# Optimization experiments

Measured on AMD Instinct MI355X. Metric: run time of the kernel, lower is better.

The kernel has to match this reference:

```python
import jax, jax.numpy as jnp
import numpy as np

G, NPG, C, H, F, L = 256, 128, 16, 128, 128, 3
N = G * NPG          # 32768 nodes
E = 524288           # 16 edges per node on average
REG, REG_C = 0.01, 0.01
LN_EPS = 1e-5


def setup_inputs() -> dict:
    key = jax.random.key(0)
    ks = jax.random.split(key, 20)
    x = jax.random.normal(ks[0], (N, F), dtype=jnp.float32)
    # edges kept within each graph so dense pooling matches to_dense_batch semantics
    epg = E // G
    offs = jnp.repeat(jnp.arange(G, dtype=jnp.int64) * NPG, epg)
    src = jax.random.randint(ks[1], (E,), 0, NPG, dtype=jnp.int64) + offs
    tgt = jax.random.randint(ks[2], (E,), 0, NPG, dtype=jnp.int64) + offs
    edge_index = jnp.stack([src, tgt])
    mask_breaks = jax.random.bernoulli(ks[3], 0.5, (E,))
    s = jax.random.uniform(ks[4], (N, C), dtype=jnp.float32)
    batch = jnp.repeat(jnp.arange(G, dtype=jnp.int64), NPG)
    sc = 1.0 / np.sqrt(H)
    Wn = jax.random.normal(ks[5], (L, H, H), dtype=jnp.float32) * sc
    bn_ = jax.random.normal(ks[6], (L, H), dtype=jnp.float32) * sc
    Wo = jax.random.normal(ks[7], (L, H, H), dtype=jnp.float32) * sc
    bo = jax.random.normal(ks[8], (L, H), dtype=jnp.float32) * sc
    Wr = jax.random.normal(ks[9], (L, H, H), dtype=jnp.float32) * sc
    ln_g = jnp.ones((L, H), dtype=jnp.float32)
    ln_b = jnp.zeros((L, H), dtype=jnp.float32)
    fln_g = jnp.ones((H,), dtype=jnp.float32)
    fln_b = jnp.zeros((H,), dtype=jnp.float32)
    lin_w = jax.random.normal(ks[10], (1, H), dtype=jnp.float32) * sc
    bias = jnp.zeros((1,), dtype=jnp.float32)
    return {"x": x, "edge_index": edge_index, "mask_breaks": mask_breaks, "s": s,
            "batch": batch, "Wn": Wn, "bn_": bn_, "Wo": Wo, "bo": bo, "Wr": Wr,
            "ln_g": ln_g, "ln_b": ln_b, "fln_g": fln_g, "fln_b": fln_b,
            "lin_w": lin_w, "bias": bias}


def _layernorm(h, g, b):
    mu = jnp.mean(h, axis=-1, keepdims=True)
    v = jnp.mean(jnp.square(h - mu), axis=-1, keepdims=True)
    return (h - mu) * jax.lax.rsqrt(v + LN_EPS) * g + b


def reference(x, edge_index, mask_breaks, s, batch, Wn, bn_, Wo, bo, Wr,
              ln_g, ln_b, fln_g, fln_b, lin_w, bias):
    src, tgt = edge_index[0], edge_index[1]
    ones_e = jnp.ones((E,), dtype=x.dtype)
    cnt = jax.ops.segment_sum(ones_e, tgt, num_segments=N)          # in-degree
    inv_cnt = (1.0 / jnp.maximum(cnt, 1.0))[:, None]
    h = x
    for i in range(L):
        x_in = h @ Wn[i].T + bn_[i]
        x_out = h @ Wo[i].T + bo[i]
        x_root = h @ Wr[i].T
        msg = jnp.where(mask_breaks[:, None], x_in[src], x_out[src])  # [E,H]
        agg = jax.ops.segment_sum(msg, tgt, num_segments=N) * inv_cnt  # mean aggr
        h = jax.nn.relu(_layernorm(agg + x_root, ln_g[i], ln_b[i]))
    # dense per-graph views (equal-size graphs, batch ids sorted -> reshape)
    xd = h.reshape(G, NPG, H)
    sd = s.reshape(G, NPG, C)
    pooled = jnp.einsum("gnc,gnh->gch", sd, xd)                      # [G,C,H]
    pooled = _layernorm(pooled, fln_g, fln_b)
    xc = pooled @ lin_w.T                                            # [G,C,1]
    col_sum = sd.sum(axis=1)                                          # [G,C]
    cmask = (col_sum > 0)[..., None]
    xc = xc * cmask.astype(xc.dtype)
    out = xc.sum(axis=1) + bias                                      # [G,1]
    reg_loss = jnp.abs(Wo).sum() + jnp.abs(bo).sum()
    denom = (cmask.astype(xc.dtype).squeeze(-1) + 1e-7).sum(axis=1, keepdims=True)
    l1_loss = (jnp.abs(xc).sum(axis=1) / denom).mean()
    losses = REG * reg_loss + REG_C * l1_loss
    return out, losses, xc
```

## Files before the change

kernel.cpp:

```cpp
#include <hip/hip_runtime.h>

#define NN   32768
#define HD   128
#define EE   524288
#define GG   256
#define EPG  2048
#define CCd  16
#define LLd  3

typedef short short8 __attribute__((ext_vector_type(8)));
typedef float f32x4 __attribute__((ext_vector_type(4)));

__device__ __forceinline__ unsigned short f2bf(float f) {
  unsigned u = __builtin_bit_cast(unsigned, f);
  return (unsigned short)((u + 0x7FFFu + ((u >> 16) & 1u)) >> 16);
}
__device__ __forceinline__ unsigned bfpack(float a, float b) {
  return (unsigned)f2bf(a) | ((unsigned)f2bf(b) << 16);
}

__global__ __launch_bounds__(256) void convert_w_kernel(const float* __restrict__ Wn, const float* __restrict__ Wo,
                                                        const float* __restrict__ Wr, const float* __restrict__ bo,
                                                        unsigned* __restrict__ Wnb, unsigned* __restrict__ Wob,
                                                        unsigned* __restrict__ Wrb, float* __restrict__ wsreg) {
  int i = blockIdx.x * 256 + threadIdx.x;
  float4 a = *(const float4*)(Wn + (size_t)i * 4);
  float4 b = *(const float4*)(Wo + (size_t)i * 4);
  float4 c = *(const float4*)(Wr + (size_t)i * 4);
  *(uint2*)(Wnb + (size_t)i * 2) = make_uint2(bfpack(a.x, a.y), bfpack(a.z, a.w));
  *(uint2*)(Wob + (size_t)i * 2) = make_uint2(bfpack(b.x, b.y), bfpack(b.z, b.w));
  *(uint2*)(Wrb + (size_t)i * 2) = make_uint2(bfpack(c.x, c.y), bfpack(c.z, c.w));
  float s = fabsf(b.x) + fabsf(b.y) + fabsf(b.z) + fabsf(b.w);
  if (blockIdx.x == 0 && threadIdx.x < 96) {
    float4 d = *(const float4*)(bo + threadIdx.x * 4);
    s += fabsf(d.x) + fabsf(d.y) + fabsf(d.z) + fabsf(d.w);
  }
#pragma unroll
  for (int mk = 1; mk < 64; mk <<= 1) s += __shfl_xor(s, mk, 64);
  if ((threadIdx.x & 63) == 0) atomicAdd(wsreg, s);
}

__global__ __launch_bounds__(256) void build_m_kernel(const int* __restrict__ src, const int* __restrict__ tgt,
                                                      const int* __restrict__ mask,
                                                      unsigned* __restrict__ Mb, float* __restrict__ fin,
                                                      float* __restrict__ fout) {
  __shared__ unsigned Mi[2 * 128 * 64];
  const int g = blockIdx.x;
  const int tid = threadIdx.x;
  for (int i = tid; i < 16384; i += 256) Mi[i] = 0;
  __syncthreads();
  const int e0 = g * EPG;
#pragma unroll
  for (int i = 0; i < 8; ++i) {
    int e = e0 + i * 256 + tid;
    int t = tgt[e] & 127;
    int sl = src[e] & 127;
    int dir = (mask[e] != 0) ? 0 : 1;
    atomicAdd(&Mi[dir * 8192 + t * 64 + (sl >> 1)], 1u << ((sl & 1) * 16));
  }
  __syncthreads();
  const int t = tid >> 1, p = tid & 1;
  unsigned nin = 0, nout = 0;
#pragma unroll 4
  for (int k = 0; k < 32; ++k) { unsigned v = Mi[t * 64 + p * 32 + k]; nin += (v & 0xffffu) + (v >> 16); }
#pragma unroll 4
  for (int k = 0; k < 32; ++k) { unsigned v = Mi[8192 + t * 64 + p * 32 + k]; nout += (v & 0xffffu) + (v >> 16); }
  nin += __shfl_xor((int)nin, 1);
  nout += __shfl_xor((int)nout, 1);
  unsigned dg = nin + nout;
  float inv = 1.0f / (float)(dg > 0 ? dg : 1);
  if (p == 0) { fin[g * 128 + t] = (float)nin * inv; fout[g * 128 + t] = (float)nout * inv; }
#pragma unroll
  for (int dir = 0; dir < 2; ++dir) {
    int base = dir * 8192 + t * 64 + p * 32;
#pragma unroll
    for (int k4 = 0; k4 < 8; ++k4) {
      uint4 v = *(const uint4*)&Mi[base + k4 * 4];
      uint4 o;
      o.x = bfpack((float)(v.x & 0xffffu) * inv, (float)(v.x >> 16) * inv);
      o.y = bfpack((float)(v.y & 0xffffu) * inv, (float)(v.y >> 16) * inv);
      o.z = bfpack((float)(v.z & 0xffffu) * inv, (float)(v.z >> 16) * inv);
      o.w = bfpack((float)(v.w & 0xffffu) * inv, (float)(v.w >> 16) * inv);
      *(uint4*)&Mb[(size_t)g * 16384 + base + k4 * 4] = o;
    }
  }
}

#define SSTR 136
#define YSTR 40
__global__ __launch_bounds__(512) void fused_kernel(
    const float* __restrict__ x, const unsigned short* __restrict__ Mb,
    const unsigned short* __restrict__ Wnb, const unsigned short* __restrict__ Wob,
    const unsigned short* __restrict__ Wrb,
    const float* __restrict__ bn, const float* __restrict__ bo,
    const float* __restrict__ fin, const float* __restrict__ fout,
    const float* __restrict__ lng, const float* __restrict__ lnb,
    const float* __restrict__ s,
    const float* __restrict__ flng, const float* __restrict__ flnb,
    const float* __restrict__ linw, const float* __restrict__ bias,
    float* __restrict__ out, float* __restrict__ l1g) {
  __shared__ unsigned short scratch[128 * SSTR];
  __shared__ unsigned short ys[2 * 128 * YSTR];
  __shared__ unsigned short sTs[16 * SSTR];
  __shared__ float colsumS[CCd];
  __shared__ float xcs[CCd], axcs[CCd], msk[CCd];

  const int g = blockIdx.x;
  const int tid = threadIdx.x;
  const int wave = tid >> 6;
  const int lane = tid & 63;
  const int m = lane & 15;
  const int q = lane >> 4;
  const unsigned short* Mg = Mb + (size_t)g * 32768;
  unsigned* scratch32 = (unsigned*)scratch;

  {
    const float4* xg = (const float4*)(x + (size_t)g * 16384);
#pragma unroll
    for (int i = 0; i < 8; ++i) {
      int flat = i * 512 + tid;
      int t = flat >> 5, f = (flat & 31) << 2;
      float4 v = xg[flat];
      int w0 = (t * SSTR + f) >> 1;
      scratch32[w0] = bfpack(v.x, v.y);
      scratch32[w0 + 1] = bfpack(v.z, v.w);
    }
    int t = tid >> 2, c0 = (tid & 3) << 2;
    float4 v = *(const float4*)(s + (size_t)g * 2048 + t * 16 + c0);
    sTs[(c0 + 0) * SSTR + t] = f2bf(v.x);
    sTs[(c0 + 1) * SSTR + t] = f2bf(v.y);
    sTs[(c0 + 2) * SSTR + t] = f2bf(v.z);
    sTs[(c0 + 3) * SSTR + t] = f2bf(v.w);
    if (tid < CCd) {
      float cs = 0.f;
      for (int tt = 0; tt < 128; ++tt) cs += s[(size_t)g * 2048 + tt * 16 + tid];
      colsumS[tid] = cs;
    }
  }
  __syncthreads();

  for (int L = 0; L < LLd; ++L) {
    const unsigned short* WnL = Wnb + (size_t)L * 16384;
    const unsigned short* WoL = Wob + (size_t)L * 16384;
    const unsigned short* WrL = Wrb + (size_t)L * 16384;
    f32x4 pre[8];
#pragma unroll
    for (int ct = 0; ct < 8; ++ct) pre[ct] = (f32x4){0.f, 0.f, 0.f, 0.f};

#pragma unroll
    for (int ks = 0; ks < 4; ++ks) {
      short8 a = *(const short8*)&scratch[(wave * 16 + m) * SSTR + ks * 32 + q * 8];
#pragma unroll
      for (int ct = 0; ct < 8; ++ct) {
        short8 b = *(const short8*)(WrL + (size_t)(ct * 16 + m) * 128 + ks * 32 + q * 8);
        pre[ct] = __builtin_amdgcn_mfma_f32_16x16x32_bf16(a, b, pre[ct], 0, 0, 0);
      }
    }

    short8 wnf[4], wof[4];
#pragma unroll
    for (int ks = 0; ks < 4; ++ks) {
      wnf[ks] = *(const short8*)(WnL + (size_t)(wave * 16 + m) * 128 + ks * 32 + q * 8);
      wof[ks] = *(const short8*)(WoL + (size_t)(wave * 16 + m) * 128 + ks * 32 + q * 8);
    }

    for (int sc = 0; sc < 4; ++sc) {
      f32x4 ya[2][2];
#pragma unroll
      for (int o2 = 0; o2 < 2; ++o2)
#pragma unroll
        for (int st = 0; st < 2; ++st) ya[o2][st] = (f32x4){0.f, 0.f, 0.f, 0.f};
#pragma unroll
      for (int ks = 0; ks < 4; ++ks) {
        short8 a0 = *(const short8*)&scratch[(sc * 32 + m) * SSTR + ks * 32 + q * 8];
        short8 a1 = *(const short8*)&scratch[(sc * 32 + 16 + m) * SSTR + ks * 32 + q * 8];
        ya[0][0] = __builtin_amdgcn_mfma_f32_16x16x32_bf16(a0, wnf[ks], ya[0][0], 0, 0, 0);
        ya[0][1] = __builtin_amdgcn_mfma_f32_16x16x32_bf16(a1, wnf[ks], ya[0][1], 0, 0, 0);
        ya[1][0] = __builtin_amdgcn_mfma_f32_16x16x32_bf16(a0, wof[ks], ya[1][0], 0, 0, 0);
        ya[1][1] = __builtin_amdgcn_mfma_f32_16x16x32_bf16(a1, wof[ks], ya[1][1], 0, 0, 0);
      }
#pragma unroll
      for (int o2 = 0; o2 < 2; ++o2)
#pragma unroll
        for (int st = 0; st < 2; ++st)
#pragma unroll
          for (int r = 0; r < 4; ++r)
            ys[o2 * 128 * YSTR + (wave * 16 + m) * YSTR + st * 16 + q * 4 + r] = f2bf(ya[o2][st][r]);
      __syncthreads();
#pragma unroll
      for (int o2 = 0; o2 < 2; ++o2) {
        short8 am = *(const short8*)(Mg + (size_t)o2 * 16384 + (size_t)(wave * 16 + m) * 128 + sc * 32 + q * 8);
#pragma unroll
        for (int ct = 0; ct < 8; ++ct) {
          short8 b = *(const short8*)&ys[o2 * 128 * YSTR + (ct * 16 + m) * YSTR + q * 8];
          pre[ct] = __builtin_amdgcn_mfma_f32_16x16x32_bf16(am, b, pre[ct], 0, 0, 0);
        }
      }
      if (sc < 3) __syncthreads();
    }

    float bnv[8], bov[8], gv[8], bv[8];
#pragma unroll
    for (int ct = 0; ct < 8; ++ct) {
      int c = L * 128 + ct * 16 + m;
      bnv[ct] = bn[c]; bov[ct] = bo[c]; gv[ct] = lng[c]; bv[ct] = lnb[c];
    }
#pragma unroll
    for (int r = 0; r < 4; ++r) {
      const int tl = q * 4 + r;
      const int T = g * 128 + wave * 16 + tl;
      const float fiv = fin[T], fov = fout[T];
      float v[8];
      float sum = 0.f;
#pragma unroll
      for (int ct = 0; ct < 8; ++ct) {
        v[ct] = pre[ct][r] + fiv * bnv[ct] + fov * bov[ct];
        sum += v[ct];
      }
      sum += __shfl_xor(sum, 1); sum += __shfl_xor(sum, 2);
      sum += __shfl_xor(sum, 4); sum += __shfl_xor(sum, 8);
      const float mu = sum * (1.0f / 128.0f);
      float sq = 0.f;
#pragma unroll
      for (int ct = 0; ct < 8; ++ct) { float d = v[ct] - mu; sq += d * d; }
      sq += __shfl_xor(sq, 1); sq += __shfl_xor(sq, 2);
      sq += __shfl_xor(sq, 4); sq += __shfl_xor(sq, 8);
      const float rstd = rsqrtf(sq * (1.0f / 128.0f) + 1e-5f);
#pragma unroll
      for (int ct = 0; ct < 8; ++ct) {
        float o = fmaxf((v[ct] - mu) * rstd * gv[ct] + bv[ct], 0.0f);
        scratch[(wave * 16 + tl) * SSTR + ct * 16 + m] = f2bf(o);
      }
    }
    __syncthreads();
  }

  f32x4 pl = (f32x4){0.f, 0.f, 0.f, 0.f};
#pragma unroll
  for (int ks = 0; ks < 4; ++ks) {
    short8 a = *(const short8*)&sTs[m * SSTR + ks * 32 + q * 8];
    short8 b;
#pragma unroll
    for (int j = 0; j < 8; ++j)
      b[j] = (short)scratch[(ks * 32 + q * 8 + j) * SSTR + wave * 16 + m];
    pl = __builtin_amdgcn_mfma_f32_16x16x32_bf16(a, b, pl, 0, 0, 0);
  }
  float* pooledS = (float*)ys;
#pragma unroll
  for (int r = 0; r < 4; ++r) pooledS[(q * 4 + r) * 132 + wave * 16 + m] = pl[r];
  __syncthreads();

  if (tid < 256) {
    const int c = tid >> 4;
    const int j0 = (tid & 15) << 3;
    float v[8];
#pragma unroll
    for (int jj = 0; jj < 8; ++jj) v[jj] = pooledS[c * 132 + j0 + jj];
    float sum = 0.f;
#pragma unroll
    for (int jj = 0; jj < 8; ++jj) sum += v[jj];
#pragma unroll
    for (int mk = 1; mk < 16; mk <<= 1) sum += __shfl_xor(sum, mk, 64);
    float mu = sum * (1.0f / 128.0f);
    float sq = 0.f;
#pragma unroll
    for (int jj = 0; jj < 8; ++jj) { float d = v[jj] - mu; sq += d * d; }
#pragma unroll
    for (int mk = 1; mk < 16; mk <<= 1) sq += __shfl_xor(sq, mk, 64);
    float rstd = rsqrtf(sq * (1.0f / 128.0f) + 1e-5f);
    float dot = 0.f;
#pragma unroll
    for (int jj = 0; jj < 8; ++jj) {
      float nv = (v[jj] - mu) * rstd * flng[j0 + jj] + flnb[j0 + jj];
      dot += nv * linw[j0 + jj];
    }
#pragma unroll
    for (int mk = 1; mk < 16; mk <<= 1) dot += __shfl_xor(dot, mk, 64);
    if ((tid & 15) == 0) {
      float cm = (colsumS[c] > 0.f) ? 1.0f : 0.0f;
      float xcv = dot * cm;
      out[257 + g * CCd + c] = xcv;
      xcs[c] = xcv; axcs[c] = fabsf(xcv); msk[c] = cm;
    }
  }
  __syncthreads();
  if (tid == 0) {
    float so = 0.f, sa = 0.f, sd = 0.f;
#pragma unroll
    for (int k = 0; k < CCd; ++k) { so += xcs[k]; sa += axcs[k]; sd += msk[k] + 1e-7f; }
    out[g] = so + bias[0];
    l1g[g] = sa / sd;
  }
}

__global__ __launch_bounds__(256) void combine_kernel(const float* __restrict__ l1g, const float* __restrict__ wsreg,
                                                      float* __restrict__ outp) {
  const int tid = threadIdx.x;
  float s2 = l1g[tid];
#pragma unroll
  for (int mk = 1; mk < 64; mk <<= 1) s2 += __shfl_xor(s2, mk, 64);
  __shared__ float rs2[4];
  if ((tid & 63) == 0) rs2[tid >> 6] = s2;
  __syncthreads();
  if (tid == 0) {
    float l1 = (rs2[0] + rs2[1] + rs2[2] + rs2[3]) * (1.0f / GG);
    outp[0] = 0.01f * wsreg[0] + 0.01f * l1;
  }
}

extern "C" void kernel_launch(void* const* d_in, const int* in_sizes, int n_in,
                              void* d_out, int out_size, void* d_ws, size_t ws_size,
                              hipStream_t stream) {
  (void)in_sizes; (void)n_in; (void)out_size; (void)ws_size;
  const float* x    = (const float*)d_in[0];
  const int*   ei   = (const int*)d_in[1];
  const int*   mask = (const int*)d_in[2];
  const float* s    = (const float*)d_in[3];
  const float* Wn   = (const float*)d_in[5];
  const float* bn   = (const float*)d_in[6];
  const float* Wo   = (const float*)d_in[7];
  const float* bo   = (const float*)d_in[8];
  const float* Wr   = (const float*)d_in[9];
  const float* lng  = (const float*)d_in[10];
  const float* lnb  = (const float*)d_in[11];
  const float* flng = (const float*)d_in[12];
  const float* flnb = (const float*)d_in[13];
  const float* linw = (const float*)d_in[14];
  const float* bias = (const float*)d_in[15];
  float* out = (float*)d_out;

  char* ws = (char*)d_ws;
  size_t off = 0;
  auto alloc = [&](size_t b) { char* p = ws + off; off += (b + 255) & ~(size_t)255; return p; };
  unsigned short* Mbuf = (unsigned short*)alloc((size_t)GG * 2 * 128 * 128 * 2);
  float* fin    = (float*)alloc((size_t)NN * 4);
  float* fout   = (float*)alloc((size_t)NN * 4);
  unsigned short* Wnb = (unsigned short*)alloc((size_t)LLd * HD * HD * 2);
  unsigned short* Wob = (unsigned short*)alloc((size_t)LLd * HD * HD * 2);
  unsigned short* Wrb = (unsigned short*)alloc((size_t)LLd * HD * HD * 2);
  float* l1g    = (float*)alloc((size_t)GG * 4);
  float* wsreg  = (float*)alloc(256);

  const int* srcA = ei;
  const int* tgtA = ei + EE;

  hipMemsetAsync(wsreg, 0, 4, stream);
  convert_w_kernel<<<LLd * HD * HD / (256 * 4), 256, 0, stream>>>(Wn, Wo, Wr, bo,
      (unsigned*)Wnb, (unsigned*)Wob, (unsigned*)Wrb, wsreg);
  build_m_kernel<<<GG, 256, 0, stream>>>(srcA, tgtA, mask, (unsigned*)Mbuf, fin, fout);
  fused_kernel<<<GG, 512, 0, stream>>>(x, Mbuf, Wnb, Wob, Wrb, bn, bo, fin, fout,
                                       lng, lnb, s, flng, flnb, linw, bias, out, l1g);
  combine_kernel<<<1, 256, 0, stream>>>(l1g, wsreg, out + 256);
}
```

Before: 163.7 us.

## Split fused GNN kernel into per-layer kernels with half-graph blocks

```diff
diff --git a/kernel.cpp b/kernel.cpp
--- a/kernel.cpp
+++ b/kernel.cpp
@@ -7,6 +7,7 @@
 #define EPG  2048
 #define CCd  16
 #define LLd  3
+#define SSTR 136
 
 typedef short short8 __attribute__((ext_vector_type(8)));
 typedef float f32x4 __attribute__((ext_vector_type(4)));
@@ -18,36 +19,39 @@
 __device__ __forceinline__ unsigned bfpack(float a, float b) {
   return (unsigned)f2bf(a) | ((unsigned)f2bf(b) << 16);
 }
-
-__global__ __launch_bounds__(256) void convert_w_kernel(const float* __restrict__ Wn, const float* __restrict__ Wo,
-                                                        const float* __restrict__ Wr, const float* __restrict__ bo,
-                                                        unsigned* __restrict__ Wnb, unsigned* __restrict__ Wob,
-                                                        unsigned* __restrict__ Wrb, float* __restrict__ wsreg) {
-  int i = blockIdx.x * 256 + threadIdx.x;
-  float4 a = *(const float4*)(Wn + (size_t)i * 4);
-  float4 b = *(const float4*)(Wo + (size_t)i * 4);
-  float4 c = *(const float4*)(Wr + (size_t)i * 4);
-  *(uint2*)(Wnb + (size_t)i * 2) = make_uint2(bfpack(a.x, a.y), bfpack(a.z, a.w));
-  *(uint2*)(Wob + (size_t)i * 2) = make_uint2(bfpack(b.x, b.y), bfpack(b.z, b.w));
-  *(uint2*)(Wrb + (size_t)i * 2) = make_uint2(bfpack(c.x, c.y), bfpack(c.z, c.w));
-  float s = fabsf(b.x) + fabsf(b.y) + fabsf(b.z) + fabsf(b.w);
-  if (blockIdx.x == 0 && threadIdx.x < 96) {
-    float4 d = *(const float4*)(bo + threadIdx.x * 4);
-    s += fabsf(d.x) + fabsf(d.y) + fabsf(d.z) + fabsf(d.w);
-  }
-#pragma unroll
-  for (int mk = 1; mk < 64; mk <<= 1) s += __shfl_xor(s, mk, 64);
-  if ((threadIdx.x & 63) == 0) atomicAdd(wsreg, s);
-}
-
-__global__ __launch_bounds__(256) void build_m_kernel(const int* __restrict__ src, const int* __restrict__ tgt,
-                                                      const int* __restrict__ mask,
-                                                      unsigned* __restrict__ Mb, float* __restrict__ fin,
-                                                      float* __restrict__ fout) {
+#define MFMA __builtin_amdgcn_mfma_f32_16x16x32_bf16
+
+__global__ __launch_bounds__(256) void prep_kernel(const int* __restrict__ src, const int* __restrict__ tgt,
+                                                   const int* __restrict__ mask,
+                                                   const float* __restrict__ Wn, const float* __restrict__ Wo,
+                                                   const float* __restrict__ Wr, const float* __restrict__ bo,
+                                                   unsigned* __restrict__ Mb, float* __restrict__ fin,
+                                                   float* __restrict__ fout,
+                                                   unsigned* __restrict__ Wnb, unsigned* __restrict__ Wob,
+                                                   unsigned* __restrict__ Wrb, float* __restrict__ wsreg) {
   __shared__ unsigned Mi[2 * 128 * 64];
+  const int tid = threadIdx.x;
+  if (blockIdx.x >= GG) {
+    int i = (blockIdx.x - GG) * 256 + tid;
+    float4 a = *(const float4*)(Wn + (size_t)i * 4);
+    float4 b = *(const float4*)(Wo + (size_t)i * 4);
+    float4 c = *(const float4*)(Wr + (size_t)i * 4);
+    *(uint2*)(Wnb + (size_t)i * 2) = make_uint2(bfpack(a.x, a.y), bfpack(a.z, a.w));
+    *(uint2*)(Wob + (size_t)i * 2) = make_uint2(bfpack(b.x, b.y), bfpack(b.z, b.w));
+    *(uint2*)(Wrb + (size_t)i * 2) = make_uint2(bfpack(c.x, c.y), bfpack(c.z, c.w));
+    float s = fabsf(b.x) + fabsf(b.y) + fabsf(b.z) + fabsf(b.w);
+    if (blockIdx.x == GG && tid < 96) {
+      float4 d = *(const float4*)(bo + tid * 4);
+      s += fabsf(d.x) + fabsf(d.y) + fabsf(d.z) + fabsf(d.w);
+    }
+#pragma unroll
+    for (int mk = 1; mk < 64; mk <<= 1) s += __shfl_xor(s, mk, 64);
+    if ((tid & 63) == 0) atomicAdd(wsreg, s);
+    return;
+  }
   const int g = blockIdx.x;
-  const int tid = threadIdx.x;
-  for (int i = tid; i < 16384; i += 256) Mi[i] = 0;
+  uint4* Mi4 = (uint4*)Mi;
+  for (int i = tid; i < 4096; i += 256) Mi4[i] = make_uint4(0, 0, 0, 0);
   __syncthreads();
   const int e0 = g * EPG;
 #pragma unroll
@@ -60,11 +64,12 @@
   }
   __syncthreads();
   const int t = tid >> 1, p = tid & 1;
+  const int b0 = t * 64 + p * 32;
   unsigned nin = 0, nout = 0;
-#pragma unroll 4
-  for (int k = 0; k < 32; ++k) { unsigned v = Mi[t * 64 + p * 32 + k]; nin += (v & 0xffffu) + (v >> 16); }
-#pragma unroll 4
-  for (int k = 0; k < 32; ++k) { unsigned v = Mi[8192 + t * 64 + p * 32 + k]; nout += (v & 0xffffu) + (v >> 16); }
+#pragma unroll 8
+  for (int k = 0; k < 32; ++k) { unsigned v = Mi[b0 + ((k + t) & 31)]; nin += (v & 0xffffu) + (v >> 16); }
+#pragma unroll 8
+  for (int k = 0; k < 32; ++k) { unsigned v = Mi[8192 + b0 + ((k + t) & 31)]; nout += (v & 0xffffu) + (v >> 16); }
   nin += __shfl_xor((int)nin, 1);
   nout += __shfl_xor((int)nout, 1);
   unsigned dg = nin + nout;
@@ -72,26 +77,174 @@
   if (p == 0) { fin[g * 128 + t] = (float)nin * inv; fout[g * 128 + t] = (float)nout * inv; }
 #pragma unroll
   for (int dir = 0; dir < 2; ++dir) {
-    int base = dir * 8192 + t * 64 + p * 32;
-#pragma unroll
-    for (int k4 = 0; k4 < 8; ++k4) {
-      uint4 v = *(const uint4*)&Mi[base + k4 * 4];
-      uint4 o;
-      o.x = bfpack((float)(v.x & 0xffffu) * inv, (float)(v.x >> 16) * inv);
-      o.y = bfpack((float)(v.y & 0xffffu) * inv, (float)(v.y >> 16) * inv);
-      o.z = bfpack((float)(v.z & 0xffffu) * inv, (float)(v.z >> 16) * inv);
-      o.w = bfpack((float)(v.w & 0xffffu) * inv, (float)(v.w >> 16) * inv);
-      *(uint4*)&Mb[(size_t)g * 16384 + base + k4 * 4] = o;
-    }
-  }
-}
-
-#define SSTR 136
-#define YSTR 40
-__global__ __launch_bounds__(512) void fused_kernel(
-    const float* __restrict__ x, const unsigned short* __restrict__ Mb,
-    const unsigned short* __restrict__ Wnb, const unsigned short* __restrict__ Wob,
-    const unsigned short* __restrict__ Wrb,
+    int base = dir * 8192 + b0;
+#pragma unroll 8
+    for (int k = 0; k < 32; ++k) {
+      int kk = (k + t) & 31;
+      unsigned v = Mi[base + kk];
+      Mb[(size_t)g * 16384 + base + kk] = bfpack((float)(v & 0xffffu) * inv, (float)(v >> 16) * inv);
+    }
+  }
+}
+
+__global__ __launch_bounds__(256, 4) void head_kernel(
+    const float* __restrict__ x,
+    const unsigned short* __restrict__ Wn0, const unsigned short* __restrict__ Wo0,
+    unsigned short* __restrict__ hOut, unsigned short* __restrict__ YtO, unsigned short* __restrict__ ZtO) {
+  __shared__ unsigned short hloc[64 * SSTR];
+  const int g = blockIdx.x >> 1, half = blockIdx.x & 1;
+  const int tid = threadIdx.x;
+  const int wave = tid >> 6, lane = tid & 63;
+  const int m = lane & 15, q = lane >> 4;
+  unsigned* hloc32 = (unsigned*)hloc;
+  const float4* xg = (const float4*)(x + (size_t)g * 16384 + (size_t)half * 8192);
+#pragma unroll
+  for (int i = 0; i < 8; ++i) {
+    int flat = i * 256 + tid;
+    int t = flat >> 5, f = (flat & 31) << 2;
+    float4 v = xg[flat];
+    int w0 = (t * SSTR + f) >> 1;
+    hloc32[w0] = bfpack(v.x, v.y);
+    hloc32[w0 + 1] = bfpack(v.z, v.w);
+  }
+  __syncthreads();
+#pragma unroll
+  for (int i = 0; i < 4; ++i) {
+    int flat = i * 256 + tid;
+    int t = flat >> 4, f = (flat & 15) << 3;
+    *(uint4*)(hOut + (size_t)g * 16384 + (size_t)(half * 64 + t) * 128 + f) =
+        *(const uint4*)&hloc[t * SSTR + f];
+  }
+  short8 afr[4];
+#pragma unroll
+  for (int ks = 0; ks < 4; ++ks)
+    afr[ks] = *(const short8*)&hloc[(wave * 16 + m) * SSTR + ks * 32 + q * 8];
+  const int srow = half * 64 + wave * 16 + q * 4;
+#pragma unroll
+  for (int ct = 0; ct < 8; ++ct) {
+    f32x4 y = (f32x4){0.f, 0.f, 0.f, 0.f}, z = (f32x4){0.f, 0.f, 0.f, 0.f};
+#pragma unroll
+    for (int ks = 0; ks < 4; ++ks) {
+      short8 bnn = *(const short8*)(Wn0 + (size_t)(ct * 16 + m) * 128 + ks * 32 + q * 8);
+      short8 boo = *(const short8*)(Wo0 + (size_t)(ct * 16 + m) * 128 + ks * 32 + q * 8);
+      y = MFMA(afr[ks], bnn, y, 0, 0, 0);
+      z = MFMA(afr[ks], boo, z, 0, 0, 0);
+    }
+    size_t o = (size_t)g * 16384 + (size_t)(ct * 16 + m) * 128 + srow;
+    *(uint2*)(YtO + o) = make_uint2(bfpack(y[0], y[1]), bfpack(y[2], y[3]));
+    *(uint2*)(ZtO + o) = make_uint2(bfpack(z[0], z[1]), bfpack(z[2], z[3]));
+  }
+}
+
+__global__ __launch_bounds__(256, 4) void mid_kernel(
+    const unsigned short* __restrict__ Mb,
+    const unsigned short* __restrict__ Yt, const unsigned short* __restrict__ Zt,
+    const unsigned short* __restrict__ hIn, const unsigned short* __restrict__ Wr,
+    const float* __restrict__ bn, const float* __restrict__ bo,
+    const float* __restrict__ fin, const float* __restrict__ fout,
+    const float* __restrict__ lng, const float* __restrict__ lnb,
+    const unsigned short* __restrict__ WnN, const unsigned short* __restrict__ WoN,
+    unsigned short* __restrict__ hOut, unsigned short* __restrict__ YtO, unsigned short* __restrict__ ZtO) {
+  __shared__ unsigned short hloc[64 * SSTR];
+  const int g = blockIdx.x >> 1, half = blockIdx.x & 1;
+  const int tid = threadIdx.x;
+  const int wave = tid >> 6, lane = tid & 63;
+  const int m = lane & 15, q = lane >> 4;
+  const int trow = half * 64 + wave * 16;
+  const unsigned short* Mg = Mb + (size_t)g * 32768;
+  const unsigned short* Ytg = Yt + (size_t)g * 16384;
+  const unsigned short* Ztg = Zt + (size_t)g * 16384;
+  const unsigned short* hg = hIn + (size_t)g * 16384;
+
+  f32x4 pre[8];
+#pragma unroll
+  for (int ct = 0; ct < 8; ++ct) pre[ct] = (f32x4){0.f, 0.f, 0.f, 0.f};
+#pragma unroll
+  for (int sc = 0; sc < 4; ++sc) {
+    short8 am0 = *(const short8*)(Mg + (size_t)(trow + m) * 128 + sc * 32 + q * 8);
+    short8 am1 = *(const short8*)(Mg + 16384 + (size_t)(trow + m) * 128 + sc * 32 + q * 8);
+#pragma unroll
+    for (int ct = 0; ct < 8; ++ct) {
+      short8 b0 = *(const short8*)(Ytg + (size_t)(ct * 16 + m) * 128 + sc * 32 + q * 8);
+      short8 b1 = *(const short8*)(Ztg + (size_t)(ct * 16 + m) * 128 + sc * 32 + q * 8);
+      pre[ct] = MFMA(am0, b0, pre[ct], 0, 0, 0);
+      pre[ct] = MFMA(am1, b1, pre[ct], 0, 0, 0);
+    }
+  }
+#pragma unroll
+  for (int ks = 0; ks < 4; ++ks) {
+    short8 a = *(const short8*)(hg + (size_t)(trow + m) * 128 + ks * 32 + q * 8);
+#pragma unroll
+    for (int ct = 0; ct < 8; ++ct) {
+      short8 b = *(const short8*)(Wr + (size_t)(ct * 16 + m) * 128 + ks * 32 + q * 8);
+      pre[ct] = MFMA(a, b, pre[ct], 0, 0, 0);
+    }
+  }
+  float bnv[8], bov[8], gv[8], bv[8];
+#pragma unroll
+  for (int ct = 0; ct < 8; ++ct) {
+    int c = ct * 16 + m;
+    bnv[ct] = bn[c]; bov[ct] = bo[c]; gv[ct] = lng[c]; bv[ct] = lnb[c];
+  }
+#pragma unroll
+  for (int r = 0; r < 4; ++r) {
+    const int T = g * 128 + trow + q * 4 + r;
+    const float fiv = fin[T], fov = fout[T];
+    float v[8];
+    float sum = 0.f;
+#pragma unroll
+    for (int ct = 0; ct < 8; ++ct) {
+      v[ct] = pre[ct][r] + fiv * bnv[ct] + fov * bov[ct];
+      sum += v[ct];
+    }
+    sum += __shfl_xor(sum, 1); sum += __shfl_xor(sum, 2);
+    sum += __shfl_xor(sum, 4); sum += __shfl_xor(sum, 8);
+    const float mu = sum * (1.0f / 128.0f);
+    float sq = 0.f;
+#pragma unroll
+    for (int ct = 0; ct < 8; ++ct) { float d = v[ct] - mu; sq += d * d; }
+    sq += __shfl_xor(sq, 1); sq += __shfl_xor(sq, 2);
+    sq += __shfl_xor(sq, 4); sq += __shfl_xor(sq, 8);
+    const float rstd = rsqrtf(sq * (1.0f / 128.0f) + 1e-5f);
+#pragma unroll
+    for (int ct = 0; ct < 8; ++ct) {
+      float o = fmaxf((v[ct] - mu) * rstd * gv[ct] + bv[ct], 0.0f);
+      hloc[(wave * 16 + q * 4 + r) * SSTR + ct * 16 + m] = f2bf(o);
+    }
+  }
+  __syncthreads();
+#pragma unroll
+  for (int i = 0; i < 4; ++i) {
+    int flat = i * 256 + tid;
+    int t = flat >> 4, f = (flat & 15) << 3;
+    *(uint4*)(hOut + (size_t)g * 16384 + (size_t)(half * 64 + t) * 128 + f) =
+        *(const uint4*)&hloc[t * SSTR + f];
+  }
+  short8 afr[4];
+#pragma unroll
+  for (int ks = 0; ks < 4; ++ks)
+    afr[ks] = *(const short8*)&hloc[(wave * 16 + m) * SSTR + ks * 32 + q * 8];
+  const int srow = half * 64 + wave * 16 + q * 4;
+#pragma unroll
+  for (int ct = 0; ct < 8; ++ct) {
+    f32x4 y = (f32x4){0.f, 0.f, 0.f, 0.f}, z = (f32x4){0.f, 0.f, 0.f, 0.f};
+#pragma unroll
+    for (int ks = 0; ks < 4; ++ks) {
+      short8 bnn = *(const short8*)(WnN + (size_t)(ct * 16 + m) * 128 + ks * 32 + q * 8);
+      short8 boo = *(const short8*)(WoN + (size_t)(ct * 16 + m) * 128 + ks * 32 + q * 8);
+      y = MFMA(afr[ks], bnn, y, 0, 0, 0);
+      z = MFMA(afr[ks], boo, z, 0, 0, 0);
+    }
+    size_t o = (size_t)g * 16384 + (size_t)(ct * 16 + m) * 128 + srow;
+    *(uint2*)(YtO + o) = make_uint2(bfpack(y[0], y[1]), bfpack(y[2], y[3]));
+    *(uint2*)(ZtO + o) = make_uint2(bfpack(z[0], z[1]), bfpack(z[2], z[3]));
+  }
+}
+
+__global__ __launch_bounds__(512, 2) void tail_kernel(
+    const unsigned short* __restrict__ Mb,
+    const unsigned short* __restrict__ Yt, const unsigned short* __restrict__ Zt,
+    const unsigned short* __restrict__ hIn, const unsigned short* __restrict__ Wr,
     const float* __restrict__ bn, const float* __restrict__ bo,
     const float* __restrict__ fin, const float* __restrict__ fout,
     const float* __restrict__ lng, const float* __restrict__ lnb,
@@ -99,32 +252,21 @@
     const float* __restrict__ flng, const float* __restrict__ flnb,
     const float* __restrict__ linw, const float* __restrict__ bias,
     float* __restrict__ out, float* __restrict__ l1g) {
-  __shared__ unsigned short scratch[128 * SSTR];
-  __shared__ unsigned short ys[2 * 128 * YSTR];
+  __shared__ unsigned short hloc[128 * SSTR];
   __shared__ unsigned short sTs[16 * SSTR];
-  __shared__ float colsumS[CCd];
-  __shared__ float xcs[CCd], axcs[CCd], msk[CCd];
-
+  __shared__ float pooledS[16 * 132];
+  __shared__ float colsumS[CCd], xcs[CCd], axcs[CCd], msk[CCd];
   const int g = blockIdx.x;
   const int tid = threadIdx.x;
-  const int wave = tid >> 6;
-  const int lane = tid & 63;
-  const int m = lane & 15;
-  const int q = lane >> 4;
+  const int wave = tid >> 6, lane = tid & 63;
+  const int m = lane & 15, q = lane >> 4;
+  const int trow = wave * 16;
   const unsigned short* Mg = Mb + (size_t)g * 32768;
-  unsigned* scratch32 = (unsigned*)scratch;
+  const unsigned short* Ytg = Yt + (size_t)g * 16384;
+  const unsigned short* Ztg = Zt + (size_t)g * 16384;
+  const unsigned short* hg = hIn + (size_t)g * 16384;
 
   {
-    const float4* xg = (const float4*)(x + (size_t)g * 16384);
-#pragma unroll
-    for (int i = 0; i < 8; ++i) {
-      int flat = i * 512 + tid;
-      int t = flat >> 5, f = (flat & 31) << 2;
-      float4 v = xg[flat];
-      int w0 = (t * SSTR + f) >> 1;
-      scratch32[w0] = bfpack(v.x, v.y);
-      scratch32[w0 + 1] = bfpack(v.z, v.w);
-    }
     int t = tid >> 2, c0 = (tid & 3) << 2;
     float4 v = *(const float4*)(s + (size_t)g * 2048 + t * 16 + c0);
     sTs[(c0 + 0) * SSTR + t] = f2bf(v.x);
@@ -137,119 +279,79 @@
       colsumS[tid] = cs;
     }
   }
-  __syncthreads();
-
-  for (int L = 0; L < LLd; ++L) {
-    const unsigned short* WnL = Wnb + (size_t)L * 16384;
-    const unsigned short* WoL = Wob + (size_t)L * 16384;
-    const unsigned short* WrL = Wrb + (size_t)L * 16384;
-    f32x4 pre[8];
-#pragma unroll
-    for (int ct = 0; ct < 8; ++ct) pre[ct] = (f32x4){0.f, 0.f, 0.f, 0.f};
-
+
+  f32x4 pre[8];
+#pragma unroll
+  for (int ct = 0; ct < 8; ++ct) pre[ct] = (f32x4){0.f, 0.f, 0.f, 0.f};
+#pragma unroll
+  for (int sc = 0; sc < 4; ++sc) {
+    short8 am0 = *(const short8*)(Mg + (size_t)(trow + m) * 128 + sc * 32 + q * 8);
+    short8 am1 = *(const short8*)(Mg + 16384 + (size_t)(trow + m) * 128 + sc * 32 + q * 8);
+#pragma unroll
+    for (int ct = 0; ct < 8; ++ct) {
+      short8 b0 = *(const short8*)(Ytg + (size_t)(ct * 16 + m) * 128 + sc * 32 + q * 8);
+      short8 b1 = *(const short8*)(Ztg + (size_t)(ct * 16 + m) * 128 + sc * 32 + q * 8);
+      pre[ct] = MFMA(am0, b0, pre[ct], 0, 0, 0);
+      pre[ct] = MFMA(am1, b1, pre[ct], 0, 0, 0);
+    }
+  }
+#pragma unroll
+  for (int ks = 0; ks < 4; ++ks) {
+    short8 a = *(const short8*)(hg + (size_t)(trow + m) * 128 + ks * 32 + q * 8);
+#pragma unroll
+    for (int ct = 0; ct < 8; ++ct) {
+      short8 b = *(const short8*)(Wr + (size_t)(ct * 16 + m) * 128 + ks * 32 + q * 8);
+      pre[ct] = MFMA(a, b, pre[ct], 0, 0, 0);
+    }
+  }
+  float bnv[8], bov[8], gv[8], bv[8];
+#pragma unroll
+  for (int ct = 0; ct < 8; ++ct) {
+    int c = ct * 16 + m;
+    bnv[ct] = bn[c]; bov[ct] = bo[c]; gv[ct] = lng[c]; bv[ct] = lnb[c];
+  }
+#pragma unroll
+  for (int r = 0; r < 4; ++r) {
+    const int T = g * 128 + trow + q * 4 + r;
+    const float fiv = fin[T], fov = fout[T];
+    float v[8];
+    float sum = 0.f;
+#pragma unroll
+    for (int ct = 0; ct < 8; ++ct) {
+      v[ct] = pre[ct][r] + fiv * bnv[ct] + fov * bov[ct];
+      sum += v[ct];
+    }
+    sum += __shfl_xor(sum, 1); sum += __shfl_xor(sum, 2);
+    sum += __shfl_xor(sum, 4); sum += __shfl_xor(sum, 8);
+    const float mu = sum * (1.0f / 128.0f);
+    float sq = 0.f;
+#pragma unroll
+    for (int ct = 0; ct < 8; ++ct) { float d = v[ct] - mu; sq += d * d; }
+    sq += __shfl_xor(sq, 1); sq += __shfl_xor(sq, 2);
+    sq += __shfl_xor(sq, 4); sq += __shfl_xor(sq, 8);
+    const float rstd = rsqrtf(sq * (1.0f / 128.0f) + 1e-5f);
+#pragma unroll
+    for (int ct = 0; ct < 8; ++ct) {
+      float o = fmaxf((v[ct] - mu) * rstd * gv[ct] + bv[ct], 0.0f);
+      hloc[(trow + q * 4 + r) * SSTR + ct * 16 + m] = f2bf(o);
+    }
+  }
+  __syncthreads();
+  {
+    f32x4 pl = (f32x4){0.f, 0.f, 0.f, 0.f};
 #pragma unroll
     for (int ks = 0; ks < 4; ++ks) {
-      short8 a = *(const short8*)&scratch[(wave * 16 + m) * SSTR + ks * 32 + q * 8];
-#pragma unroll
-      for (int ct = 0; ct < 8; ++ct) {
-        short8 b = *(const short8*)(WrL + (size_t)(ct * 16 + m) * 128 + ks * 32 + q * 8);
-        pre[ct] = __builtin_amdgcn_mfma_f32_16x16x32_bf16(a, b, pre[ct], 0, 0, 0);
-      }
-    }
-
-    short8 wnf[4], wof[4];
-#pragma unroll
-    for (int ks = 0; ks < 4; ++ks) {
-      wnf[ks] = *(const short8*)(WnL + (size_t)(wave * 16 + m) * 128 + ks * 32 + q * 8);
-      wof[ks] = *(const short8*)(WoL + (size_t)(wave * 16 + m) * 128 + ks * 32 + q * 8);
-    }
-
-    for (int sc = 0; sc < 4; ++sc) {
-      f32x4 ya[2][2];
-#pragma unroll
-      for (int o2 = 0; o2 < 2; ++o2)
-#pragma unroll
-        for (int st = 0; st < 2; ++st) ya[o2][st] = (f32x4){0.f, 0.f, 0.f, 0.f};
-#pragma unroll
-      for (int ks = 0; ks < 4; ++ks) {
-        short8 a0 = *(const short8*)&scratch[(sc * 32 + m) * SSTR + ks * 32 + q * 8];
-        short8 a1 = *(const short8*)&scratch[(sc * 32 + 16 + m) * SSTR + ks * 32 + q * 8];
-        ya[0][0] = __builtin_amdgcn_mfma_f32_16x16x32_bf16(a0, wnf[ks], ya[0][0], 0, 0, 0);
-        ya[0][1] = __builtin_amdgcn_mfma_f32_16x16x32_bf16(a1, wnf[ks], ya[0][1], 0, 0, 0);
-        ya[1][0] = __builtin_amdgcn_mfma_f32_16x16x32_bf16(a0, wof[ks], ya[1][0], 0, 0, 0);
-        ya[1][1] = __builtin_amdgcn_mfma_f32_16x16x32_bf16(a1, wof[ks], ya[1][1], 0, 0, 0);
-      }
-#pragma unroll
-      for (int o2 = 0; o2 < 2; ++o2)
-#pragma unroll
-        for (int st = 0; st < 2; ++st)
-#pragma unroll
-          for (int r = 0; r < 4; ++r)
-            ys[o2 * 128 * YSTR + (wave * 16 + m) * YSTR + st * 16 + q * 4 + r] = f2bf(ya[o2][st][r]);
-      __syncthreads();
-#pragma unroll
-      for (int o2 = 0; o2 < 2; ++o2) {
-        short8 am = *(const short8*)(Mg + (size_t)o2 * 16384 + (size_t)(wave * 16 + m) * 128 + sc * 32 + q * 8);
-#pragma unroll
-        for (int ct = 0; ct < 8; ++ct) {
-          short8 b = *(const short8*)&ys[o2 * 128 * YSTR + (ct * 16 + m) * YSTR + q * 8];
-          pre[ct] = __builtin_amdgcn_mfma_f32_16x16x32_bf16(am, b, pre[ct], 0, 0, 0);
-        }
-      }
-      if (sc < 3) __syncthreads();
-    }
-
-    float bnv[8], bov[8], gv[8], bv[8];
-#pragma unroll
-    for (int ct = 0; ct < 8; ++ct) {
-      int c = L * 128 + ct * 16 + m;
-      bnv[ct] = bn[c]; bov[ct] = bo[c]; gv[ct] = lng[c]; bv[ct] = lnb[c];
-    }
-#pragma unroll
-    for (int r = 0; r < 4; ++r) {
-      const int tl = q * 4 + r;
-      const int T = g * 128 + wave * 16 + tl;
-      const float fiv = fin[T], fov = fout[T];
-      float v[8];
-      float sum = 0.f;
-#pragma unroll
-      for (int ct = 0; ct < 8; ++ct) {
-        v[ct] = pre[ct][r] + fiv * bnv[ct] + fov * bov[ct];
-        sum += v[ct];
-      }
-      sum += __shfl_xor(sum, 1); sum += __shfl_xor(sum, 2);
-      sum += __shfl_xor(sum, 4); sum += __shfl_xor(sum, 8);
-      const float mu = sum * (1.0f / 128.0f);
-      float sq = 0.f;
-#pragma unroll
-      for (int ct = 0; ct < 8; ++ct) { float d = v[ct] - mu; sq += d * d; }
-      sq += __shfl_xor(sq, 1); sq += __shfl_xor(sq, 2);
-      sq += __shfl_xor(sq, 4); sq += __shfl_xor(sq, 8);
-      const float rstd = rsqrtf(sq * (1.0f / 128.0f) + 1e-5f);
-#pragma unroll
-      for (int ct = 0; ct < 8; ++ct) {
-        float o = fmaxf((v[ct] - mu) * rstd * gv[ct] + bv[ct], 0.0f);
-        scratch[(wave * 16 + tl) * SSTR + ct * 16 + m] = f2bf(o);
-      }
-    }
-    __syncthreads();
-  }
-
-  f32x4 pl = (f32x4){0.f, 0.f, 0.f, 0.f};
-#pragma unroll
-  for (int ks = 0; ks < 4; ++ks) {
-    short8 a = *(const short8*)&sTs[m * SSTR + ks * 32 + q * 8];
-    short8 b;
-#pragma unroll
-    for (int j = 0; j < 8; ++j)
-      b[j] = (short)scratch[(ks * 32 + q * 8 + j) * SSTR + wave * 16 + m];
-    pl = __builtin_amdgcn_mfma_f32_16x16x32_bf16(a, b, pl, 0, 0, 0);
-  }
-  float* pooledS = (float*)ys;
-#pragma unroll
-  for (int r = 0; r < 4; ++r) pooledS[(q * 4 + r) * 132 + wave * 16 + m] = pl[r];
-  __syncthreads();
-
+      short8 a = *(const short8*)&sTs[m * SSTR + ks * 32 + q * 8];
+      short8 b;
+#pragma unroll
+      for (int j = 0; j < 8; ++j)
+        b[j] = (short)hloc[(ks * 32 + q * 8 + j) * SSTR + wave * 16 + m];
+      pl = MFMA(a, b, pl, 0, 0, 0);
+    }
+#pragma unroll
+    for (int r = 0; r < 4; ++r) pooledS[(q * 4 + r) * 132 + wave * 16 + m] = pl[r];
+  }
+  __syncthreads();
   if (tid < 256) {
     const int c = tid >> 4;
     const int j0 = (tid & 15) << 3;
@@ -338,6 +440,12 @@
   unsigned short* Wnb = (unsigned short*)alloc((size_t)LLd * HD * HD * 2);
   unsigned short* Wob = (unsigned short*)alloc((size_t)LLd * HD * HD * 2);
   unsigned short* Wrb = (unsigned short*)alloc((size_t)LLd * HD * HD * 2);
+  unsigned short* hA  = (unsigned short*)alloc((size_t)NN * HD * 2);
+  unsigned short* hB  = (unsigned short*)alloc((size_t)NN * HD * 2);
+  unsigned short* YtA = (unsigned short*)alloc((size_t)NN * HD * 2);
+  unsigned short* ZtA = (unsigned short*)alloc((size_t)NN * HD * 2);
+  unsigned short* YtB = (unsigned short*)alloc((size_t)NN * HD * 2);
+  unsigned short* ZtB = (unsigned short*)alloc((size_t)NN * HD * 2);
   float* l1g    = (float*)alloc((size_t)GG * 4);
   float* wsreg  = (float*)alloc(256);
 
@@ -345,10 +453,14 @@
   const int* tgtA = ei + EE;
 
   hipMemsetAsync(wsreg, 0, 4, stream);
-  convert_w_kernel<<<LLd * HD * HD / (256 * 4), 256, 0, stream>>>(Wn, Wo, Wr, bo,
-      (unsigned*)Wnb, (unsigned*)Wob, (unsigned*)Wrb, wsreg);
-  build_m_kernel<<<GG, 256, 0, stream>>>(srcA, tgtA, mask, (unsigned*)Mbuf, fin, fout);
-  fused_kernel<<<GG, 512, 0, stream>>>(x, Mbuf, Wnb, Wob, Wrb, bn, bo, fin, fout,
-                                       lng, lnb, s, flng, flnb, linw, bias, out, l1g);
+  prep_kernel<<<GG + 48, 256, 0, stream>>>(srcA, tgtA, mask, Wn, Wo, Wr, bo,
+      (unsigned*)Mbuf, fin, fout, (unsigned*)Wnb, (unsigned*)Wob, (unsigned*)Wrb, wsreg);
+  head_kernel<<<2 * GG, 256, 0, stream>>>(x, Wnb, Wob, hA, YtA, ZtA);
+  mid_kernel<<<2 * GG, 256, 0, stream>>>(Mbuf, YtA, ZtA, hA, Wrb,
+      bn, bo, fin, fout, lng, lnb, Wnb + 16384, Wob + 16384, hB, YtB, ZtB);
+  mid_kernel<<<2 * GG, 256, 0, stream>>>(Mbuf, YtB, ZtB, hB, Wrb + 16384,
+      bn + 128, bo + 128, fin, fout, lng + 128, lnb + 128, Wnb + 32768, Wob + 32768, hA, YtA, ZtA);
+  tail_kernel<<<GG, 512, 0, stream>>>(Mbuf, YtA, ZtA, hA, Wrb + 32768,
+      bn + 256, bo + 256, fin, fout, lng + 256, lnb + 256, s, flng, flnb, linw, bias, out, l1g);
   combine_kernel<<<1, 256, 0, stream>>>(l1g, wsreg, out + 256);
 }
```

Result: slower. 264.9 us (+61.9%).
